# Kernel tuning notes

Measured on AMD Instinct MI355X. Metric: run time of the kernel, lower is better.

The kernel has to match this reference:

```python
import jax, jax.numpy as jnp
import numpy as np

B, S, H = 2, 2048, 2048
NH, NKV, HD = 32, 8, 64          # num_heads, num_kv_heads, head_dim
G = NH // NKV                     # GQA group size
NEG = -1e9


def setup_inputs() -> dict:
    key = jax.random.key(0)
    ks = jax.random.split(key, 8)
    x = jax.random.normal(ks[0], (B, S, H), dtype=jnp.float32)
    # real RoPE frequencies: theta = 10000 ** (-2i/hd)
    inv_freq = 1.0 / (10000.0 ** (np.arange(0, HD, 2, dtype=np.float32) / HD))
    angles = np.arange(S, dtype=np.float32)[:, None] * inv_freq[None, :]  # [S, HD//2]
    freqs_cos = jnp.asarray(np.cos(angles))
    freqs_sin = jnp.asarray(np.sin(angles))
    # additive causal mask [S, S]
    mask = jnp.where(jnp.tril(jnp.ones((S, S), dtype=bool)), 0.0, NEG).astype(jnp.float32)
    sc = 0.02
    Wq = jax.random.normal(ks[1], (NH * HD, H), dtype=jnp.float32) * sc
    bq = jax.random.normal(ks[2], (NH * HD,), dtype=jnp.float32) * sc
    Wk = jax.random.normal(ks[3], (NKV * HD, H), dtype=jnp.float32) * sc
    bk = jax.random.normal(ks[4], (NKV * HD,), dtype=jnp.float32) * sc
    Wv = jax.random.normal(ks[5], (NKV * HD, H), dtype=jnp.float32) * sc
    bv = jax.random.normal(ks[6], (NKV * HD,), dtype=jnp.float32) * sc
    Wo = jax.random.normal(ks[7], (H, NH * HD), dtype=jnp.float32) * sc
    return {"x": x, "freqs_cos": freqs_cos, "freqs_sin": freqs_sin, "mask": mask,
            "Wq": Wq, "bq": bq, "Wk": Wk, "bk": bk, "Wv": Wv, "bv": bv, "Wo": Wo}


def _rotate_half(t):
    h = t.shape[-1] // 2
    return jnp.concatenate([-t[..., h:], t[..., :h]], axis=-1)


def reference(x, freqs_cos, freqs_sin, mask, Wq, bq, Wk, bk, Wv, bv, Wo):
    b, s, _ = x.shape
    q = (x @ Wq.T + bq).reshape(b, s, NH, HD)
    k = (x @ Wk.T + bk).reshape(b, s, NKV, HD)
    v = (x @ Wv.T + bv).reshape(b, s, NKV, HD)
    # RoPE (rotate_half style): cos/sin duplicated along last dim -> [1, s, 1, HD]
    cos = jnp.concatenate([freqs_cos, freqs_cos], axis=-1)[None, :, None, :]
    sin = jnp.concatenate([freqs_sin, freqs_sin], axis=-1)[None, :, None, :]
    q = q * cos + _rotate_half(q) * sin
    k = k * cos + _rotate_half(k) * sin
    # GQA: view q as [b, s, NKV, G, HD]; avoids repeat_interleave of K/V (same math)
    q5 = q.reshape(b, s, NKV, G, HD)
    scores = jnp.einsum('bqhgd,bkhd->bhgqk', q5, k) / jnp.sqrt(jnp.float32(HD))
    scores = scores + mask  # broadcast [s, s] over [b, h, g, s, s]
    p = jax.nn.softmax(scores.astype(jnp.float32), axis=-1).astype(q.dtype)
    out = jnp.einsum('bhgqk,bkhd->bqhgd', p, v).reshape(b, s, NH * HD)
    return out @ Wo.T
```

## Files before the change

kernel.cpp:

```cpp
#include <hip/hip_runtime.h>
#include <hip/hip_bf16.h>
#include <cstddef>
#include <cstdint>

#define B_   2
#define S_   2048
#define H_   2048
#define NH_  32
#define NKV_ 8
#define HD_  64

typedef __attribute__((ext_vector_type(8))) short short8;
typedef __attribute__((ext_vector_type(4))) float v4f;
typedef __attribute__((ext_vector_type(16))) float v16f;

#define MAXC 48.0f
#define QSCALE 0.18033688011112042f

__device__ __forceinline__ unsigned short f2b(float f) {
    unsigned int u = __float_as_uint(f);
    u += 0x7FFFu + ((u >> 16) & 1u);
    return (unsigned short)(u >> 16);
}
__device__ __forceinline__ unsigned int pkbf(float a, float b) {
    __hip_bfloat162 h = __float22bfloat162_rn(float2{a, b});
    return *(unsigned int*)&h;
}
__device__ __forceinline__ float fexp2(float x) {
#if __has_builtin(__builtin_amdgcn_exp2f)
    return __builtin_amdgcn_exp2f(x);
#else
    return exp2f(x);
#endif
}
__device__ __forceinline__ v4f mfma16(short8 a, short8 b, v4f c) {
    return __builtin_amdgcn_mfma_f32_16x16x32_bf16(a, b, c, 0, 0, 0);
}
__device__ __forceinline__ v16f mfma32(short8 a, short8 b, v16f c) {
    return __builtin_amdgcn_mfma_f32_32x32x16_bf16(a, b, c, 0, 0, 0);
}
__device__ __forceinline__ void gll16(void* lds, const void* g) {
    __builtin_amdgcn_global_load_lds(
        (const __attribute__((address_space(1))) unsigned int*)g,
        (__attribute__((address_space(3))) unsigned int*)lds, 16, 0, 0);
}

__global__ __launch_bounds__(256) void convert_all(
    const float* __restrict__ x, const float* __restrict__ wq,
    const float* __restrict__ wk, const float* __restrict__ wv,
    const float* __restrict__ wo,
    unsigned short* __restrict__ xb, unsigned short* __restrict__ wqb,
    unsigned short* __restrict__ wkb, unsigned short* __restrict__ wvb,
    unsigned short* __restrict__ wob)
{
    size_t i = ((size_t)blockIdx.x * 256 + threadIdx.x) * 4;
    const float* src; unsigned short* dst; size_t off;
    if (i < 8388608)       { src = x;  dst = xb;  off = i; }
    else if (i < 12582912) { src = wq; dst = wqb; off = i - 8388608; }
    else if (i < 13631488) { src = wk; dst = wkb; off = i - 12582912; }
    else if (i < 14680064) { src = wv; dst = wvb; off = i - 13631488; }
    else                   { src = wo; dst = wob; off = i - 14680064; }
    float4 v = *(const float4*)(src + off);
    ushort4 o;
    o.x = f2b(v.x); o.y = f2b(v.y); o.z = f2b(v.z); o.w = f2b(v.w);
    *(ushort4*)(dst + off) = o;
}

__global__ __launch_bounds__(512, 2) void qkv_gemm(
    const unsigned short* __restrict__ xb,
    const unsigned short* __restrict__ wqb, const unsigned short* __restrict__ wkb,
    const unsigned short* __restrict__ wvb,
    const float* __restrict__ bq, const float* __restrict__ bk,
    const float* __restrict__ bv,
    const float* __restrict__ fc, const float* __restrict__ fs,
    unsigned short* __restrict__ Qb, unsigned short* __restrict__ Kb,
    unsigned short* __restrict__ Vt)
{
    __shared__ unsigned short As[2][256 * 64];
    __shared__ unsigned short Bs[2][256 * 64];
    const int tid = threadIdx.x;
    const int lane = tid & 63, w = tid >> 6;
    const int tx = lane & 15, quad = lane >> 4;

    const int bid = blockIdx.x;
    const int swz = (bid & 7) * 24 + (bid >> 3);
    const int bi = swz / 12, bj = swz % 12;
    const int bm = bi * 256, bcol = bj * 256;

    const unsigned short* Bp; int mode, nbase;
    if (bj < 8)       { Bp = wqb + (size_t)bcol * 2048;          mode = 0; nbase = bcol; }
    else if (bj < 10) { Bp = wkb + (size_t)(bcol - 2048) * 2048; mode = 1; nbase = bcol - 2048; }
    else              { Bp = wvb + (size_t)(bcol - 2560) * 2048; mode = 2; nbase = bcol - 2560; }
    const unsigned short* Ap = xb + (size_t)bm * 2048;

    const int wm = (w >> 2) * 128, wn = (w & 3) * 64;

    v4f acc[8][4];
#pragma unroll
    for (int i = 0; i < 8; ++i)
#pragma unroll
        for (int j = 0; j < 4; ++j) acc[i][j] = (v4f)0.f;

    const int r8 = lane >> 3, gc = (lane & 7) ^ r8;
    const unsigned short* ga = Ap + (size_t)(w * 32 + r8) * 2048 + gc * 8;
    const unsigned short* gb = Bp + (size_t)(w * 32 + r8) * 2048 + gc * 8;

#define QKV_STAGE(c, t) { \
    _Pragma("unroll") \
    for (int i_ = 0; i_ < 4; ++i_) { \
        gll16(&As[c][(w * 32 + i_ * 8) * 64], ga + (size_t)(i_ * 8) * 2048 + (t) * 64); \
        gll16(&Bs[c][(w * 32 + i_ * 8) * 64], gb + (size_t)(i_ * 8) * 2048 + (t) * 64); \
    } }

    const int t7 = tx & 7;
    int sl[2];
#pragma unroll
    for (int kk = 0; kk < 2; ++kk) sl[kk] = ((kk * 4 + quad) ^ t7) * 8;

    QKV_STAGE(0, 0)
    QKV_STAGE(1, 1)

    for (int t = 0; t < 32; ++t) {
        if (t < 31) asm volatile("s_waitcnt vmcnt(8)" ::: "memory");
        else        asm volatile("s_waitcnt vmcnt(0)" ::: "memory");
        __builtin_amdgcn_sched_barrier(0);
        __builtin_amdgcn_s_barrier();
        __builtin_amdgcn_sched_barrier(0);

        const unsigned short* Asb = As[t & 1];
        const unsigned short* Bsb = Bs[t & 1];
#pragma unroll
        for (int kk = 0; kk < 2; ++kk) {
            short8 bfr[4];
#pragma unroll
            for (int nt = 0; nt < 4; ++nt)
                bfr[nt] = *(const short8*)&Bsb[(wn + nt * 16 + tx) * 64 + sl[kk]];
            __builtin_amdgcn_s_setprio(1);
#pragma unroll
            for (int mt = 0; mt < 8; ++mt) {
                short8 a = *(const short8*)&Asb[(wm + mt * 16 + tx) * 64 + sl[kk]];
#pragma unroll
                for (int nt = 0; nt < 4; ++nt)
                    acc[mt][nt] = mfma16(a, bfr[nt], acc[mt][nt]);
            }
            __builtin_amdgcn_s_setprio(0);
        }

        __builtin_amdgcn_sched_barrier(0);
        __builtin_amdgcn_s_barrier();
        __builtin_amdgcn_sched_barrier(0);
        if (t < 30) QKV_STAGE(t & 1, t + 2)
    }
#undef QKV_STAGE

    if (mode <= 1) {
        unsigned short* Cout = mode ? Kb : Qb;
        const float* bias    = mode ? bk : bq;
        const int ldN        = mode ? 512 : 2048;
        const float scq      = mode ? 1.0f : QSCALE;
        float bx0 = bias[nbase + wn +  0 + tx];
        float bx1 = bias[nbase + wn + 16 + tx];
        float bx2 = bias[nbase + wn + 32 + tx];
        float bx3 = bias[nbase + wn + 48 + tx];
#pragma unroll
        for (int mt = 0; mt < 8; ++mt)
#pragma unroll
            for (int rg = 0; rg < 4; ++rg) {
                int m = bm + wm + mt * 16 + quad * 4 + rg;
                int s = m & (S_ - 1);
                float c0 = fc[s * 32 + tx],      c1 = fc[s * 32 + 16 + tx];
                float s0 = fs[s * 32 + tx],      s1 = fs[s * 32 + 16 + tx];
                float q0 = acc[mt][0][rg] + bx0, q1 = acc[mt][1][rg] + bx1;
                float q2 = acc[mt][2][rg] + bx2, q3 = acc[mt][3][rg] + bx3;
                size_t base = (size_t)m * ldN + nbase + wn + tx;
                Cout[base]      = f2b((q0 * c0 - q2 * s0) * scq);
                Cout[base + 16] = f2b((q1 * c1 - q3 * s1) * scq);
                Cout[base + 32] = f2b((q2 * c0 + q0 * s0) * scq);
                Cout[base + 48] = f2b((q3 * c1 + q1 * s1) * scq);
            }
    } else {
#pragma unroll
        for (int nt = 0; nt < 4; ++nt) {
            int d = nbase + wn + nt * 16 + tx;
            float bvv = bv[d];
#pragma unroll
            for (int mt = 0; mt < 8; ++mt) {
                int m0 = bm + wm + mt * 16 + quad * 4;
                ushort4 o;
                o.x = f2b(acc[mt][nt][0] + bvv);
                o.y = f2b(acc[mt][nt][1] + bvv);
                o.z = f2b(acc[mt][nt][2] + bvv);
                o.w = f2b(acc[mt][nt][3] + bvv);
                *(ushort4*)&Vt[(size_t)d * 4096 + m0] = o;
            }
        }
    }
}

__global__ __launch_bounds__(256) void out_gemm(
    const unsigned short* __restrict__ Ab, const unsigned short* __restrict__ Bw,
    float* __restrict__ C)
{
    __shared__ unsigned short As[128 * 64];
    __shared__ unsigned short Bs[128 * 64];
    const int tid = threadIdx.x;
    const int lane = tid & 63, w = tid >> 6;
    const int tx = lane & 15, quad = lane >> 4;
    const int bm = blockIdx.y * 128, bn = blockIdx.x * 128;
    const int wm = (w >> 1) * 64, wn = (w & 1) * 64;

    v4f acc[4][4];
#pragma unroll
    for (int i = 0; i < 4; ++i)
#pragma unroll
        for (int j = 0; j < 4; ++j) acc[i][j] = (v4f)0.f;

    const int r8 = lane >> 3, gc = (lane & 7) ^ r8;
    const unsigned short* ga = &Ab[(size_t)(bm + w * 32 + r8) * 2048 + gc * 8];
    const unsigned short* gb = &Bw[(size_t)(bn + w * 32 + r8) * 2048 + gc * 8];
    const int t7 = tx & 7;
    int sl[2];
#pragma unroll
    for (int kk = 0; kk < 2; ++kk) sl[kk] = ((kk * 4 + quad) ^ t7) * 8;

    for (int k0 = 0; k0 < 2048; k0 += 64) {
        __syncthreads();
#pragma unroll
        for (int i = 0; i < 4; ++i) {
            gll16(&As[(w * 32 + i * 8) * 64], ga + (size_t)(i * 8) * 2048 + k0);
            gll16(&Bs[(w * 32 + i * 8) * 64], gb + (size_t)(i * 8) * 2048 + k0);
        }
        __syncthreads();
#pragma unroll
        for (int kk = 0; kk < 2; ++kk) {
            short8 af[4], bf[4];
#pragma unroll
            for (int mt = 0; mt < 4; ++mt)
                af[mt] = *(const short8*)&As[(wm + mt * 16 + tx) * 64 + sl[kk]];
#pragma unroll
            for (int nt = 0; nt < 4; ++nt)
                bf[nt] = *(const short8*)&Bs[(wn + nt * 16 + tx) * 64 + sl[kk]];
#pragma unroll
            for (int mt = 0; mt < 4; ++mt)
#pragma unroll
                for (int nt = 0; nt < 4; ++nt)
                    acc[mt][nt] = mfma16(af[mt], bf[nt], acc[mt][nt]);
        }
    }
#pragma unroll
    for (int mt = 0; mt < 4; ++mt)
#pragma unroll
        for (int nt = 0; nt < 4; ++nt)
#pragma unroll
            for (int rg = 0; rg < 4; ++rg) {
                int m = bm + wm + mt * 16 + quad * 4 + rg;
                C[(size_t)m * 2048 + bn + wn + nt * 16 + tx] = acc[mt][nt][rg];
            }
}

__global__ __launch_bounds__(256, 4) void attn_mfma(
    const unsigned short* __restrict__ Q, const unsigned short* __restrict__ K,
    const unsigned short* __restrict__ Vt, unsigned short* __restrict__ O)
{
    __shared__ __align__(16) unsigned short smem[2][2][64 * 72];
    const int tid = threadIdx.x;
    const int lane = tid & 63, wq = tid >> 6;
    const int l32 = lane & 31, half = lane >> 5;
    const int qh = wq & 1;
    const int ts = wq >> 1;
    const int p = blockIdx.x;
    const int h = blockIdx.y, b = blockIdx.z;
    const int kvh = h >> 2;

    const int srow = tid >> 3, sc8 = (tid & 7) * 8;
    const unsigned short* gkB = &K[(((size_t)b * S_ + srow) * NKV_ + kvh) * HD_ + sc8];
    const unsigned short* gvB = &Vt[(size_t)(kvh * 64 + srow) * 4096 + (size_t)b * 2048 + sc8];
    const int woff = srow * 72 + sc8;

    for (int ph = 0; ph < 2; ++ph) {
        const int T = ph ? (31 - p) : p;

        const int qrow = T * 64 + qh * 32 + l32;
        const unsigned short* Qr = &Q[(((size_t)b * S_ + qrow) * NH_ + h) * HD_];
        short8 qf[4];
#pragma unroll
        for (int s = 0; s < 4; ++s)
            qf[s] = *(const short8*)(Qr + s * 16 + half * 8);

        float la = 0.f, lb = 0.f, lc = 0.f, ld = 0.f;
        v16f o0 = (v16f)0.f, o1 = (v16f)0.f;

        uint4 kr0 = *(const uint4*)(gkB);
        uint4 kr1 = *(const uint4*)(gkB + 32 * (NKV_ * HD_));
        uint4 vr0 = *(const uint4*)(gvB);
        uint4 vr1 = *(const uint4*)(gvB + (size_t)32 * 4096);
        int cur = 0;

        for (int kt = 0; kt <= T; ++kt) {
            unsigned short* Kw = &smem[cur][0][woff];
            unsigned short* Vw = &smem[cur][1][woff];
            *(uint4*)(Kw)           = kr0;
            *(uint4*)(Kw + 32 * 72) = kr1;
            *(uint4*)(Vw)           = vr0;
            *(uint4*)(Vw + 32 * 72) = vr1;
            __syncthreads();
            if (kt < T) {
                const unsigned short* gk = gkB + (size_t)(kt + 1) * 64 * (NKV_ * HD_);
                const unsigned short* gv = gvB + (kt + 1) * 64;
                kr0 = *(const uint4*)(gk);
                kr1 = *(const uint4*)(gk + 32 * (NKV_ * HD_));
                vr0 = *(const uint4*)(gv);
                vr1 = *(const uint4*)(gv + (size_t)32 * 4096);
            }
            const unsigned short* Ksb = smem[cur][0];
            const unsigned short* Vsb = smem[cur][1];
            cur ^= 1;

            const bool diag = (kt == T);
            if (diag && ts > qh) continue;
            const bool part = diag && (ts == qh);

            const int kb = (ts * 32 + l32) * 72 + half * 8;
            v16f st = (v16f)(-MAXC);
            __builtin_amdgcn_s_setprio(1);
            st = mfma32(*(const short8*)&Ksb[kb],      qf[0], st);
            st = mfma32(*(const short8*)&Ksb[kb + 16], qf[1], st);
            st = mfma32(*(const short8*)&Ksb[kb + 32], qf[2], st);
            st = mfma32(*(const short8*)&Ksb[kb + 48], qf[3], st);
            __builtin_amdgcn_s_setprio(0);

            float pv[16];
#pragma unroll
            for (int r = 0; r < 16; ++r) pv[r] = fexp2(st[r]);
            if (part) {
#pragma unroll
                for (int r = 0; r < 16; ++r) {
                    int krow = (r & 3) + 8 * (r >> 2) + 4 * half;
                    if (krow > l32) pv[r] = 0.f;
                }
            }
            la += (pv[0]  + pv[1])  + (pv[2]  + pv[3]);
            lb += (pv[4]  + pv[5])  + (pv[6]  + pv[7]);
            lc += (pv[8]  + pv[9])  + (pv[10] + pv[11]);
            ld += (pv[12] + pv[13]) + (pv[14] + pv[15]);

            unsigned int u[8];
#pragma unroll
            for (int g = 0; g < 4; ++g) {
                u[2 * g]     = pkbf(pv[4 * g],     pv[4 * g + 1]);
                u[2 * g + 1] = pkbf(pv[4 * g + 2], pv[4 * g + 3]);
            }
#pragma unroll
            for (int sg = 0; sg < 2; ++sg) {
                unsigned int a0 = u[4 * sg], a1 = u[4 * sg + 1];
                unsigned int b0 = u[4 * sg + 2], b1 = u[4 * sg + 3];
                uint4 fw;
#if __has_builtin(__builtin_amdgcn_permlane32_swap)
                typedef unsigned int u2v __attribute__((ext_vector_type(2)));
                u2v r0 = __builtin_amdgcn_permlane32_swap(a0, b0, false, false);
                u2v r1 = __builtin_amdgcn_permlane32_swap(a1, b1, false, false);
                fw.x = r0[0]; fw.y = r1[0]; fw.z = r0[1]; fw.w = r1[1];
#else
                unsigned int s0 = __shfl_xor((int)a0, 32);
                unsigned int s1 = __shfl_xor((int)a1, 32);
                unsigned int s2 = __shfl_xor((int)b0, 32);
                unsigned int s3 = __shfl_xor((int)b1, 32);
                fw.x = half ? s2 : a0;
                fw.y = half ? s3 : a1;
                fw.z = half ? b0 : s0;
                fw.w = half ? b1 : s1;
#endif
                short8 pf = *(short8*)&fw;
                const int vo = (2 * ts + sg) * 16 + half * 8;
                __builtin_amdgcn_s_setprio(1);
                o0 = mfma32(*(const short8*)&Vsb[l32 * 72 + vo],        pf, o0);
                o1 = mfma32(*(const short8*)&Vsb[(32 + l32) * 72 + vo], pf, o1);
                __builtin_amdgcn_s_setprio(0);
            }
        }

        float l = (la + lb) + (lc + ld);
        l += __shfl_xor(l, 32);

        __syncthreads();
        float* red = (float*)&smem[0][0][0];
        const int rbase = (qh * 64 + lane) * 33;
        if (ts == 1) {
#pragma unroll
            for (int r = 0; r < 16; ++r) { red[rbase + r] = o0[r]; red[rbase + 16 + r] = o1[r]; }
            red[rbase + 32] = l;
        }
        __syncthreads();
        if (ts == 0) {
#pragma unroll
            for (int r = 0; r < 16; ++r) { o0[r] += red[rbase + r]; o1[r] += red[rbase + 16 + r]; }
            l += red[rbase + 32];
            float inv = 1.f / l;
            int qg = T * 64 + qh * 32 + l32;
            unsigned short* orow = &O[((size_t)b * S_ + qg) * (NH_ * HD_) + h * HD_];
#pragma unroll
            for (int td = 0; td < 2; ++td) {
                const v16f& oo = td ? o1 : o0;
#pragma unroll
                for (int g = 0; g < 4; ++g) {
                    int d = td * 32 + g * 8 + half * 4;
                    uint2 uu;
                    uu.x = pkbf(oo[4 * g] * inv,     oo[4 * g + 1] * inv);
                    uu.y = pkbf(oo[4 * g + 2] * inv, oo[4 * g + 3] * inv);
                    *(uint2*)&orow[d] = uu;
                }
            }
        }
        if (ph == 0) __syncthreads();
    }
}

extern "C" void kernel_launch(void* const* d_in, const int* in_sizes, int n_in,
                              void* d_out, int out_size, void* d_ws, size_t ws_size,
                              hipStream_t stream)
{
    const float* x  = (const float*)d_in[0];
    const float* fc = (const float*)d_in[1];
    const float* fs = (const float*)d_in[2];
    const float* Wq = (const float*)d_in[4];
    const float* bq = (const float*)d_in[5];
    const float* Wk = (const float*)d_in[6];
    const float* bk = (const float*)d_in[7];
    const float* Wv = (const float*)d_in[8];
    const float* bv = (const float*)d_in[9];
    const float* Wo = (const float*)d_in[10];
    float* out = (float*)d_out;

    unsigned short* ws = (unsigned short*)d_ws;
    unsigned short* xb  = ws;
    unsigned short* wqb = ws + 8388608;
    unsigned short* wkb = ws + 12582912;
    unsigned short* wvb = ws + 13631488;
    unsigned short* wob = ws + 14680064;
    unsigned short* Qb  = ws + 18874368;
    unsigned short* Kb  = ws + 27262976;
    unsigned short* Vt  = ws + 29360128;
    unsigned short* Ob  = ws + 31457280;

    dim3 blk(256);
    convert_all<<<18432, blk, 0, stream>>>(x, Wq, Wk, Wv, Wo, xb, wqb, wkb, wvb, wob);
    qkv_gemm<<<192, dim3(512), 0, stream>>>(xb, wqb, wkb, wvb, bq, bk, bv,
                                            fc, fs, Qb, Kb, Vt);
    attn_mfma<<<dim3(16, NH_, B_), blk, 0, stream>>>(Qb, Kb, Vt, Ob);
    out_gemm<<<dim3(16, 32), blk, 0, stream>>>(Ob, wob, out);
}
```

Before: 310.9 us.

## Triple-buffer GEMM tiles with split-phase prefetch in QKV and output projections

```diff
diff --git a/kernel.cpp b/kernel.cpp
--- a/kernel.cpp
+++ b/kernel.cpp
@@ -66,6 +66,12 @@
     *(ushort4*)(dst + off) = o;
 }
 
+
+#define STG_A(c, i, t) gll16(&As[c][(w * 32 + (i) * 8) * 64], \
+                             ga + (size_t)((i) * 8) * 2048 + (size_t)(t) * 64);
+#define STG_B(c, i, t) gll16(&Bs[c][(w * 16 + (i) * 8) * 64], \
+                             gb + (size_t)((i) * 8) * 2048 + (size_t)(t) * 64);
+
 __global__ __launch_bounds__(512, 2) void qkv_gemm(
     const unsigned short* __restrict__ xb,
     const unsigned short* __restrict__ wqb, const unsigned short* __restrict__ wkb,
@@ -76,82 +82,100 @@
     unsigned short* __restrict__ Qb, unsigned short* __restrict__ Kb,
     unsigned short* __restrict__ Vt)
 {
-    __shared__ unsigned short As[2][256 * 64];
-    __shared__ unsigned short Bs[2][256 * 64];
+    __shared__ unsigned short As[3][256 * 64];
+    __shared__ unsigned short Bs[3][128 * 64];
     const int tid = threadIdx.x;
     const int lane = tid & 63, w = tid >> 6;
     const int tx = lane & 15, quad = lane >> 4;
 
     const int bid = blockIdx.x;
-    const int swz = (bid & 7) * 24 + (bid >> 3);
-    const int bi = swz / 12, bj = swz % 12;
-    const int bm = bi * 256, bcol = bj * 256;
+    const int swz = (bid & 7) * 48 + (bid >> 3);
+    const int bi = swz / 24, bj = swz % 24;
+    const int bm = bi * 256;
 
     const unsigned short* Bp; int mode, nbase;
-    if (bj < 8)       { Bp = wqb + (size_t)bcol * 2048;          mode = 0; nbase = bcol; }
-    else if (bj < 10) { Bp = wkb + (size_t)(bcol - 2048) * 2048; mode = 1; nbase = bcol - 2048; }
-    else              { Bp = wvb + (size_t)(bcol - 2560) * 2048; mode = 2; nbase = bcol - 2560; }
+    if (bj < 16)      { Bp = wqb + (size_t)(bj * 128) * 2048;        mode = 0; nbase = bj * 128; }
+    else if (bj < 20) { Bp = wkb + (size_t)((bj - 16) * 128) * 2048; mode = 1; nbase = (bj - 16) * 128; }
+    else              { Bp = wvb + (size_t)((bj - 20) * 128) * 2048; mode = 2; nbase = (bj - 20) * 128; }
     const unsigned short* Ap = xb + (size_t)bm * 2048;
 
-    const int wm = (w >> 2) * 128, wn = (w & 3) * 64;
-
-    v4f acc[8][4];
-#pragma unroll
-    for (int i = 0; i < 8; ++i)
+    const int wm = (w >> 1) * 64, wn = (w & 1) * 64;
+
+    v4f acc[4][4];
+#pragma unroll
+    for (int i = 0; i < 4; ++i)
 #pragma unroll
         for (int j = 0; j < 4; ++j) acc[i][j] = (v4f)0.f;
 
     const int r8 = lane >> 3, gc = (lane & 7) ^ r8;
     const unsigned short* ga = Ap + (size_t)(w * 32 + r8) * 2048 + gc * 8;
-    const unsigned short* gb = Bp + (size_t)(w * 32 + r8) * 2048 + gc * 8;
-
-#define QKV_STAGE(c, t) { \
-    _Pragma("unroll") \
-    for (int i_ = 0; i_ < 4; ++i_) { \
-        gll16(&As[c][(w * 32 + i_ * 8) * 64], ga + (size_t)(i_ * 8) * 2048 + (t) * 64); \
-        gll16(&Bs[c][(w * 32 + i_ * 8) * 64], gb + (size_t)(i_ * 8) * 2048 + (t) * 64); \
-    } }
+    const unsigned short* gb = Bp + (size_t)(w * 16 + r8) * 2048 + gc * 8;
 
     const int t7 = tx & 7;
     int sl[2];
 #pragma unroll
     for (int kk = 0; kk < 2; ++kk) sl[kk] = ((kk * 4 + quad) ^ t7) * 8;
 
-    QKV_STAGE(0, 0)
-    QKV_STAGE(1, 1)
-
+    STG_A(0, 0, 0) STG_A(0, 1, 0) STG_B(0, 0, 0)
+    STG_A(0, 2, 0) STG_A(0, 3, 0) STG_B(0, 1, 0)
+    STG_A(1, 0, 1) STG_A(1, 1, 1) STG_B(1, 0, 1)
+    STG_A(1, 2, 1) STG_A(1, 3, 1) STG_B(1, 1, 1)
+
+    int cb = 0;
     for (int t = 0; t < 32; ++t) {
-        if (t < 31) asm volatile("s_waitcnt vmcnt(8)" ::: "memory");
+        if (t < 31) asm volatile("s_waitcnt vmcnt(6)" ::: "memory");
         else        asm volatile("s_waitcnt vmcnt(0)" ::: "memory");
         __builtin_amdgcn_sched_barrier(0);
         __builtin_amdgcn_s_barrier();
         __builtin_amdgcn_sched_barrier(0);
 
-        const unsigned short* Asb = As[t & 1];
-        const unsigned short* Bsb = Bs[t & 1];
-#pragma unroll
-        for (int kk = 0; kk < 2; ++kk) {
-            short8 bfr[4];
-#pragma unroll
-            for (int nt = 0; nt < 4; ++nt)
-                bfr[nt] = *(const short8*)&Bsb[(wn + nt * 16 + tx) * 64 + sl[kk]];
-            __builtin_amdgcn_s_setprio(1);
-#pragma unroll
-            for (int mt = 0; mt < 8; ++mt) {
-                short8 a = *(const short8*)&Asb[(wm + mt * 16 + tx) * 64 + sl[kk]];
-#pragma unroll
-                for (int nt = 0; nt < 4; ++nt)
-                    acc[mt][nt] = mfma16(a, bfr[nt], acc[mt][nt]);
-            }
-            __builtin_amdgcn_s_setprio(0);
-        }
-
+        const unsigned short* Asb = As[cb];
+        const unsigned short* Bsb = Bs[cb];
+        const int nb = (cb == 0) ? 2 : cb - 1;
+        const bool pf = (t < 30);
+
+        short8 af[4][2], bf[2][2];
+#pragma unroll
+        for (int mt = 0; mt < 4; ++mt)
+#pragma unroll
+            for (int kk = 0; kk < 2; ++kk)
+                af[mt][kk] = *(const short8*)&Asb[(wm + mt * 16 + tx) * 64 + sl[kk]];
+#pragma unroll
+        for (int nt = 0; nt < 2; ++nt)
+#pragma unroll
+            for (int kk = 0; kk < 2; ++kk)
+                bf[nt][kk] = *(const short8*)&Bsb[(wn + nt * 16 + tx) * 64 + sl[kk]];
+        if (pf) { STG_A(nb, 0, t + 2) STG_A(nb, 1, t + 2) STG_B(nb, 0, t + 2) }
+        __builtin_amdgcn_s_setprio(1);
+#pragma unroll
+        for (int kk = 0; kk < 2; ++kk)
+#pragma unroll
+            for (int mt = 0; mt < 4; ++mt)
+#pragma unroll
+                for (int nt = 0; nt < 2; ++nt)
+                    acc[mt][nt] = mfma16(af[mt][kk], bf[nt][kk], acc[mt][nt]);
+        __builtin_amdgcn_s_setprio(0);
         __builtin_amdgcn_sched_barrier(0);
         __builtin_amdgcn_s_barrier();
         __builtin_amdgcn_sched_barrier(0);
-        if (t < 30) QKV_STAGE(t & 1, t + 2)
+
+#pragma unroll
+        for (int nt = 0; nt < 2; ++nt)
+#pragma unroll
+            for (int kk = 0; kk < 2; ++kk)
+                bf[nt][kk] = *(const short8*)&Bsb[(wn + (nt + 2) * 16 + tx) * 64 + sl[kk]];
+        if (pf) { STG_A(nb, 2, t + 2) STG_A(nb, 3, t + 2) STG_B(nb, 1, t + 2) }
+        __builtin_amdgcn_s_setprio(1);
+#pragma unroll
+        for (int kk = 0; kk < 2; ++kk)
+#pragma unroll
+            for (int mt = 0; mt < 4; ++mt)
+#pragma unroll
+                for (int nt = 0; nt < 2; ++nt)
+                    acc[mt][nt + 2] = mfma16(af[mt][kk], bf[nt][kk], acc[mt][nt + 2]);
+        __builtin_amdgcn_s_setprio(0);
+        cb = (cb == 2) ? 0 : cb + 1;
     }
-#undef QKV_STAGE
 
     if (mode <= 1) {
         unsigned short* Cout = mode ? Kb : Qb;
@@ -163,7 +187,7 @@
         float bx2 = bias[nbase + wn + 32 + tx];
         float bx3 = bias[nbase + wn + 48 + tx];
 #pragma unroll
-        for (int mt = 0; mt < 8; ++mt)
+        for (int mt = 0; mt < 4; ++mt)
 #pragma unroll
             for (int rg = 0; rg < 4; ++rg) {
                 int m = bm + wm + mt * 16 + quad * 4 + rg;
@@ -184,7 +208,7 @@
             int d = nbase + wn + nt * 16 + tx;
             float bvv = bv[d];
 #pragma unroll
-            for (int mt = 0; mt < 8; ++mt) {
+            for (int mt = 0; mt < 4; ++mt) {
                 int m0 = bm + wm + mt * 16 + quad * 4;
                 ushort4 o;
                 o.x = f2b(acc[mt][nt][0] + bvv);
@@ -197,16 +221,20 @@
     }
 }
 
-__global__ __launch_bounds__(256) void out_gemm(
+__global__ __launch_bounds__(512, 2) void out_gemm(
     const unsigned short* __restrict__ Ab, const unsigned short* __restrict__ Bw,
     float* __restrict__ C)
 {
-    __shared__ unsigned short As[128 * 64];
-    __shared__ unsigned short Bs[128 * 64];
+    __shared__ unsigned short As[3][256 * 64];
+    __shared__ unsigned short Bs[3][128 * 64];
     const int tid = threadIdx.x;
     const int lane = tid & 63, w = tid >> 6;
     const int tx = lane & 15, quad = lane >> 4;
-    const int bm = blockIdx.y * 128, bn = blockIdx.x * 128;
+
+    const int bid = blockIdx.x;
+    const int swz = (bid & 7) * 32 + (bid >> 3);
+    const int bm = (swz >> 4) * 256, bn = (swz & 15) * 128;
+
     const int wm = (w >> 1) * 64, wn = (w & 1) * 64;
 
     v4f acc[4][4];
@@ -216,37 +244,75 @@
         for (int j = 0; j < 4; ++j) acc[i][j] = (v4f)0.f;
 
     const int r8 = lane >> 3, gc = (lane & 7) ^ r8;
-    const unsigned short* ga = &Ab[(size_t)(bm + w * 32 + r8) * 2048 + gc * 8];
-    const unsigned short* gb = &Bw[(size_t)(bn + w * 32 + r8) * 2048 + gc * 8];
+    const unsigned short* ga = Ab + (size_t)(bm + w * 32 + r8) * 2048 + gc * 8;
+    const unsigned short* gb = Bw + (size_t)(bn + w * 16 + r8) * 2048 + gc * 8;
+
     const int t7 = tx & 7;
     int sl[2];
 #pragma unroll
     for (int kk = 0; kk < 2; ++kk) sl[kk] = ((kk * 4 + quad) ^ t7) * 8;
 
-    for (int k0 = 0; k0 < 2048; k0 += 64) {
-        __syncthreads();
-#pragma unroll
-        for (int i = 0; i < 4; ++i) {
-            gll16(&As[(w * 32 + i * 8) * 64], ga + (size_t)(i * 8) * 2048 + k0);
-            gll16(&Bs[(w * 32 + i * 8) * 64], gb + (size_t)(i * 8) * 2048 + k0);
-        }
-        __syncthreads();
-#pragma unroll
-        for (int kk = 0; kk < 2; ++kk) {
-            short8 af[4], bf[4];
+    STG_A(0, 0, 0) STG_A(0, 1, 0) STG_B(0, 0, 0)
+    STG_A(0, 2, 0) STG_A(0, 3, 0) STG_B(0, 1, 0)
+    STG_A(1, 0, 1) STG_A(1, 1, 1) STG_B(1, 0, 1)
+    STG_A(1, 2, 1) STG_A(1, 3, 1) STG_B(1, 1, 1)
+
+    int cb = 0;
+    for (int t = 0; t < 32; ++t) {
+        if (t < 31) asm volatile("s_waitcnt vmcnt(6)" ::: "memory");
+        else        asm volatile("s_waitcnt vmcnt(0)" ::: "memory");
+        __builtin_amdgcn_sched_barrier(0);
+        __builtin_amdgcn_s_barrier();
+        __builtin_amdgcn_sched_barrier(0);
+
+        const unsigned short* Asb = As[cb];
+        const unsigned short* Bsb = Bs[cb];
+        const int nb = (cb == 0) ? 2 : cb - 1;
+        const bool pf = (t < 30);
+
+        short8 af[4][2], bf[2][2];
+#pragma unroll
+        for (int mt = 0; mt < 4; ++mt)
+#pragma unroll
+            for (int kk = 0; kk < 2; ++kk)
+                af[mt][kk] = *(const short8*)&Asb[(wm + mt * 16 + tx) * 64 + sl[kk]];
+#pragma unroll
+        for (int nt = 0; nt < 2; ++nt)
+#pragma unroll
+            for (int kk = 0; kk < 2; ++kk)
+                bf[nt][kk] = *(const short8*)&Bsb[(wn + nt * 16 + tx) * 64 + sl[kk]];
+        if (pf) { STG_A(nb, 0, t + 2) STG_A(nb, 1, t + 2) STG_B(nb, 0, t + 2) }
+        __builtin_amdgcn_s_setprio(1);
+#pragma unroll
+        for (int kk = 0; kk < 2; ++kk)
 #pragma unroll
             for (int mt = 0; mt < 4; ++mt)
-                af[mt] = *(const short8*)&As[(wm + mt * 16 + tx) * 64 + sl[kk]];
-#pragma unroll
-            for (int nt = 0; nt < 4; ++nt)
-                bf[nt] = *(const short8*)&Bs[(wn + nt * 16 + tx) * 64 + sl[kk]];
+#pragma unroll
+                for (int nt = 0; nt < 2; ++nt)
+                    acc[mt][nt] = mfma16(af[mt][kk], bf[nt][kk], acc[mt][nt]);
+        __builtin_amdgcn_s_setprio(0);
+        __builtin_amdgcn_sched_barrier(0);
+        __builtin_amdgcn_s_barrier();
+        __builtin_amdgcn_sched_barrier(0);
+
+#pragma unroll
+        for (int nt = 0; nt < 2; ++nt)
+#pragma unroll
+            for (int kk = 0; kk < 2; ++kk)
+                bf[nt][kk] = *(const short8*)&Bsb[(wn + (nt + 2) * 16 + tx) * 64 + sl[kk]];
+        if (pf) { STG_A(nb, 2, t + 2) STG_A(nb, 3, t + 2) STG_B(nb, 1, t + 2) }
+        __builtin_amdgcn_s_setprio(1);
+#pragma unroll
+        for (int kk = 0; kk < 2; ++kk)
 #pragma unroll
             for (int mt = 0; mt < 4; ++mt)
 #pragma unroll
-                for (int nt = 0; nt < 4; ++nt)
-                    acc[mt][nt] = mfma16(af[mt], bf[nt], acc[mt][nt]);
-        }
+                for (int nt = 0; nt < 2; ++nt)
+                    acc[mt][nt + 2] = mfma16(af[mt][kk], bf[nt][kk], acc[mt][nt + 2]);
+        __builtin_amdgcn_s_setprio(0);
+        cb = (cb == 2) ? 0 : cb + 1;
     }
+
 #pragma unroll
     for (int mt = 0; mt < 4; ++mt)
 #pragma unroll
@@ -444,8 +510,8 @@
 
     dim3 blk(256);
     convert_all<<<18432, blk, 0, stream>>>(x, Wq, Wk, Wv, Wo, xb, wqb, wkb, wvb, wob);
-    qkv_gemm<<<192, dim3(512), 0, stream>>>(xb, wqb, wkb, wvb, bq, bk, bv,
+    qkv_gemm<<<384, dim3(512), 0, stream>>>(xb, wqb, wkb, wvb, bq, bk, bv,
                                             fc, fs, Qb, Kb, Vt);
     attn_mfma<<<dim3(16, NH_, B_), blk, 0, stream>>>(Qb, Kb, Vt, Ob);
-    out_gemm<<<dim3(16, 32), blk, 0, stream>>>(Ob, wob, out);
-}
+    out_gemm<<<256, dim3(512), 0, stream>>>(Ob, wob, out);
+}
```

New measurement: 298.3 us. -4.0%, faster.
